# Kernel optimization log

Measured on AMD Instinct MI355X. Metric: run time of the kernel, lower is better.

The kernel has to match this reference:

```python
import jax, jax.numpy as jnp
import numpy as np

D_MODEL = 512; D_INNER = 1024; D_STATE = 16; DT_RANK = 32; D_CONV = 4
N_LAYERS = 2; LSPP = 7; N_ROI = 2048; HIDDEN = 4096


def layer_norm(x, g, b, eps=1e-5):
    mu = x.mean(-1, keepdims=True)
    v = ((x - mu) ** 2).mean(-1, keepdims=True)
    return (x - mu) * jax.lax.rsqrt(v + eps) * g + b


def causal_dwconv(u, w, b):
    # u: [N,L,Di], w: [Di,K] depthwise, causal left-pad K-1
    x = jnp.transpose(u, (0, 2, 1))
    out = jax.lax.conv_general_dilated(x, w[:, None, :], (1,), [(D_CONV - 1, 0)],
                                       dimension_numbers=('NCH', 'OIH', 'NCH'),
                                       feature_group_count=D_INNER)
    return jnp.transpose(out, (0, 2, 1)) + b


def selective_scan(u, dt, A, B, C):
    # u, dt: [N,L,Di]; B, C: [N,L,S]; A: [Di,S]
    def step(h, xs):
        dt_t, B_t, C_t, u_t = xs
        dA = jnp.exp(dt_t[..., None] * A)                      # [N,Di,S]
        h = dA * h + (dt_t * u_t)[..., None] * B_t[:, None, :]
        return h, jnp.einsum('nds,ns->nd', h, C_t)
    h0 = jnp.zeros((u.shape[0], D_INNER, D_STATE), u.dtype)
    xs = (jnp.moveaxis(dt, 1, 0), jnp.moveaxis(B, 1, 0),
          jnp.moveaxis(C, 1, 0), jnp.moveaxis(u, 1, 0))
    _, ys = jax.lax.scan(step, h0, xs)
    return jnp.moveaxis(ys, 0, 1)                              # [N,L,Di]


def mamba_block(h, inw, cw, cb, xpw, dtw, dtb, Alog, Dp, ow):
    # decomposed bidirectional mamba ('dbm'): shared in_proj/gate, fwd+bwd scans summed
    xz = h @ inw.T                                             # [N,L,2*Di]
    xi, z = jnp.split(xz, 2, axis=-1)
    ys = []
    for d in range(2):
        u = xi if d == 0 else jnp.flip(xi, axis=1)
        u = jax.nn.silu(causal_dwconv(u, cw[d], cb[d]))
        dbl = u @ xpw[d].T                                     # [N,L,DT_RANK+2S]
        dtr = dbl[..., :DT_RANK]
        B = dbl[..., DT_RANK:DT_RANK + D_STATE]
        C = dbl[..., DT_RANK + D_STATE:]
        dt = jax.nn.softplus(dtr @ dtw[d].T + dtb[d])
        A = -jnp.exp(Alog[d])
        yd = selective_scan(u, dt, A, B, C) + u * Dp[d]
        ys.append(yd if d == 0 else jnp.flip(yd, axis=1))
    return ((ys[0] + ys[1]) * jax.nn.silu(z)) @ ow.T


def setup_inputs() -> dict:
    key = jax.random.key(0)
    ks = iter(jax.random.split(key, 40))
    rn = lambda shape, scale: jax.random.normal(next(ks), shape, dtype=jnp.float32) * scale
    inp = {}
    inp['x_flat'] = rn((N_ROI, D_MODEL * LSPP), 1.0)
    inp['conv_a_w'] = rn((256, 512, 3), (512 * 3) ** -0.5)
    inp['conv_p_w'] = rn((256, 512, 1), 512 ** -0.5)
    inp['se_w1'] = rn((32, 512), 512 ** -0.5)
    inp['se_b1'] = jnp.zeros((32,), jnp.float32)
    inp['se_w2'] = rn((512, 32), 32 ** -0.5)
    inp['se_b2'] = jnp.zeros((512,), jnp.float32)
    inp['ln_g'] = jnp.ones((N_LAYERS, D_MODEL), jnp.float32)
    inp['ln_b'] = jnp.zeros((N_LAYERS, D_MODEL), jnp.float32)
    inp['in_proj_w'] = rn((N_LAYERS, 2 * D_INNER, D_MODEL), D_MODEL ** -0.5)
    inp['conv_w'] = rn((N_LAYERS, 2, D_INNER, D_CONV), D_CONV ** -0.5)
    inp['conv_b'] = jnp.zeros((N_LAYERS, 2, D_INNER), jnp.float32)
    inp['x_proj_w'] = rn((N_LAYERS, 2, DT_RANK + 2 * D_STATE, D_INNER), D_INNER ** -0.5)
    inp['dt_proj_w'] = rn((N_LAYERS, 2, D_INNER, DT_RANK), DT_RANK ** -0.5)
    inp['dt_proj_b'] = rn((N_LAYERS, 2, D_INNER), 0.1) - 4.0
    inp['A_log'] = jnp.log(jnp.arange(1., D_STATE + 1., dtype=jnp.float32)) * jnp.ones((N_LAYERS, 2, D_INNER, D_STATE), jnp.float32)
    inp['D_param'] = jnp.ones((N_LAYERS, 2, D_INNER), jnp.float32)
    inp['out_proj_w'] = rn((N_LAYERS, D_MODEL, D_INNER), D_INNER ** -0.5)
    inp['out_ln_g'] = jnp.ones((D_MODEL,), jnp.float32)
    inp['out_ln_b'] = jnp.zeros((D_MODEL,), jnp.float32)
    inp['mlp_w1'] = rn((HIDDEN, D_MODEL), D_MODEL ** -0.5)
    inp['mlp_b1'] = jnp.zeros((HIDDEN,), jnp.float32)
    inp['mlp_w2'] = rn((HIDDEN, HIDDEN), HIDDEN ** -0.5)
    inp['mlp_b2'] = jnp.zeros((HIDDEN,), jnp.float32)
    return inp


def reference(x_flat, conv_a_w, conv_p_w, se_w1, se_b1, se_w2, se_b2, ln_g, ln_b,
              in_proj_w, conv_w, conv_b, x_proj_w, dt_proj_w, dt_proj_b, A_log,
              D_param, out_proj_w, out_ln_g, out_ln_b, mlp_w1, mlp_b1, mlp_w2, mlp_b2):
    N = x_flat.shape[0]
    x = x_flat.reshape(N, D_MODEL, LSPP)                       # [N,512,7]
    dn = ('NCH', 'OIH', 'NCH')
    # TSSE: strided conv branch + maxpool branch, concat, SE gating; L: 7 -> 4
    a = jax.nn.relu(jax.lax.conv_general_dilated(x, conv_a_w, (2,), [(1, 1)], dimension_numbers=dn))
    p = jax.lax.reduce_window(x, -jnp.inf, jax.lax.max, (1, 1, 3), (1, 1, 2), ((0, 0), (0, 0), (1, 1)))
    p = jax.nn.relu(jax.lax.conv_general_dilated(p, conv_p_w, (1,), [(0, 0)], dimension_numbers=dn))
    y = jnp.concatenate([a, p], axis=1)                        # [N,512,4]
    s = jax.nn.sigmoid(jax.nn.relu(y.mean(-1) @ se_w1.T + se_b1) @ se_w2.T + se_b2)
    y = y * s[:, :, None]
    # Mamba backbone: 2 pre-norm residual DBM blocks (mask is all-ones -> no-op)
    h = jnp.transpose(y, (0, 2, 1))                            # [N,L,512]
    for l in range(N_LAYERS):
        h = h + mamba_block(layer_norm(h, ln_g[l], ln_b[l]), in_proj_w[l], conv_w[l],
                            conv_b[l], x_proj_w[l], dt_proj_w[l], dt_proj_b[l],
                            A_log[l], D_param[l], out_proj_w[l])
    h = layer_norm(h, out_ln_g, out_ln_b)
    feat = h.mean(1)                                           # mean pool over time
    z1 = jax.nn.relu(feat @ mlp_w1.T + mlp_b1)
    return jax.nn.relu(z1 @ mlp_w2.T + mlp_b2)                 # [N,4096]
```

## Files before the change

kernel.cpp:

```cpp
#include <hip/hip_runtime.h>
#include <hip/hip_bf16.h>

typedef __hip_bfloat16 bf16;
typedef __attribute__((ext_vector_type(8))) short s16x8;
typedef __attribute__((ext_vector_type(4))) float f32x4;

__device__ __forceinline__ float u2f(unsigned short u){
  union { unsigned int i; float f; } v; v.i = ((unsigned int)u) << 16; return v.f;
}
__device__ __forceinline__ float bfu(bf16 x){ return __bfloat162float(x); }
__device__ __forceinline__ bf16  f2b(float x){ return __float2bfloat16(x); }

__device__ __forceinline__ void gload16(const void* g, void* l){
  __builtin_amdgcn_global_load_lds(
      (const __attribute__((address_space(1))) void*)g,
      (__attribute__((address_space(3))) void*)l, 16, 0, 0);
}

__device__ __forceinline__ float block_sum256(float v, float* red){
  #pragma unroll
  for (int o = 32; o > 0; o >>= 1) v += __shfl_down(v, o, 64);
  int lane = threadIdx.x & 63, wid = threadIdx.x >> 6;
  if (lane == 0) red[wid] = v;
  __syncthreads();
  float r = red[0] + red[1] + red[2] + red[3];
  __syncthreads();
  return r;
}

__device__ __forceinline__ ushort4 cvt4(float4 v){
  ushort4 o;
  o.x = __bfloat16_as_ushort(f2b(v.x));
  o.y = __bfloat16_as_ushort(f2b(v.y));
  o.z = __bfloat16_as_ushort(f2b(v.z));
  o.w = __bfloat16_as_ushort(f2b(v.w));
  return o;
}

__global__ __launch_bounds__(256) void prep_kernel(
    const float* __restrict__ caw, const float* __restrict__ cpw,
    const float* __restrict__ ipw, const float* __restrict__ opw,
    const float* __restrict__ xpw, const float* __restrict__ dtw,
    const float* __restrict__ alog,
    bf16* __restrict__ wa, bf16* __restrict__ wp,
    bf16* __restrict__ wbi, bf16* __restrict__ wbo,
    bf16* __restrict__ wxp, bf16* __restrict__ wdtp,
    float* __restrict__ atab)
{
  for (int i = blockIdx.x*256 + threadIdx.x; i < 1769472; i += gridDim.x*256){
    if (i < 917504){
      int j = i;
      const float4* src; ushort4* dst;
      if (j < 98304)      { src = (const float4*)caw; dst = (ushort4*)wa; }
      else if (j < 131072){ j -= 98304;  src = (const float4*)cpw; dst = (ushort4*)wp; }
      else if (j < 655360){ j -= 131072; src = (const float4*)ipw; dst = (ushort4*)wbi; }
      else                { j -= 655360; src = (const float4*)opw; dst = (ushort4*)wbo; }
      dst[j] = cvt4(src[j]);
    } else if (i < 1441792){
      int idx = i - 917504;
      int l = idx >> 18, rem = idx & 262143, row = rem >> 10, c = rem & 1023;
      int d = row >> 7, r = row & 127;
      float v = (r < 64) ? xpw[(((size_t)l*2 + d)*64 + r)*1024 + c] : 0.f;
      wxp[idx] = f2b(v);
    } else if (i < 1703936){
      int idx = i - 1441792;
      int ld = idx >> 16, rem = idx & 65535, r = rem >> 6, cc = rem & 63;
      float v = (cc < 32) ? dtw[((size_t)ld*1024 + r)*32 + cc] : 0.f;
      wdtp[idx] = f2b(v);
    } else {
      int idx = i - 1703936;
      atab[idx] = -__expf(alog[idx]) * 1.44269504088896f;
    }
  }
}

__global__ __launch_bounds__(256) void mlpprep_kernel(
    const float4* __restrict__ w1, const float4* __restrict__ w2,
    ushort4* __restrict__ o1, ushort4* __restrict__ o2)
{
  for (int i = blockIdx.x*256 + threadIdx.x; i < 4718592; i += gridDim.x*256){
    if (i < 524288) o1[i] = cvt4(w1[i]);
    else            o2[i - 524288] = cvt4(w2[i - 524288]);
  }
}

template<int ACT, int OMODE, bool HASBIAS>
__global__ __launch_bounds__(256) void mgemm_kernel(
    const bf16* __restrict__ A, const bf16* __restrict__ W,
    const float* __restrict__ bias, void* __restrict__ outp,
    int K, int ldo)
{
  __shared__ char lsA[16384];
  __shared__ char lsB[16384];
  const int tid = threadIdx.x;
  const int w = tid >> 6, l = tid & 63;
  const int nwg = gridDim.x * gridDim.y;
  const int lin = blockIdx.y * gridDim.x + blockIdx.x;
  const int cpx = nwg >> 3;
  const int swz = (lin & 7) * cpx + (lin >> 3);
  const int m0 = (swz % gridDim.x) * 128, n0 = (swz / gridDim.x) * 128;
  const int wr = w >> 1, wc = w & 1;
  const size_t ldb = (size_t)K * 2;
  const char* Ab = (const char*)A + (size_t)m0 * ldb;
  const char* Wb = (const char*)W + (size_t)n0 * ldb;

  const int srow = l >> 3;
  const int scb  = ((l & 7) ^ srow) << 4;
  const int fr = l & 15;
  const int fg = l >> 4;
  const int fsw = (fr & 7) << 4;

  f32x4 acc[4][4];
  #pragma unroll
  for (int m = 0; m < 4; ++m)
    #pragma unroll
    for (int n = 0; n < 4; ++n) acc[m][n] = (f32x4){0.f,0.f,0.f,0.f};

  const int nk = K >> 6;
  for (int kt = 0; kt < nk; ++kt){
    const char* As = Ab + (size_t)kt * 128;
    const char* Ws = Wb + (size_t)kt * 128;
    #pragma unroll
    for (int i = 0; i < 4; ++i){
      int row = (i*4 + w)*8 + srow;
      gload16(As + (size_t)row*ldb + scb, &lsA[(i*4 + w)*1024]);
    }
    #pragma unroll
    for (int i = 0; i < 4; ++i){
      int row = (i*4 + w)*8 + srow;
      gload16(Ws + (size_t)row*ldb + scb, &lsB[(i*4 + w)*1024]);
    }
    __syncthreads();

    s16x8 af[4][2], bfr[4][2];
    #pragma unroll
    for (int m = 0; m < 4; ++m){
      int row = wr*64 + m*16 + fr;
      af[m][0] = *(const s16x8*)&lsA[row*128 + (( 0 + fg*16) ^ fsw)];
      af[m][1] = *(const s16x8*)&lsA[row*128 + ((64 + fg*16) ^ fsw)];
    }
    #pragma unroll
    for (int n = 0; n < 4; ++n){
      int row = wc*64 + n*16 + fr;
      bfr[n][0] = *(const s16x8*)&lsB[row*128 + (( 0 + fg*16) ^ fsw)];
      bfr[n][1] = *(const s16x8*)&lsB[row*128 + ((64 + fg*16) ^ fsw)];
    }
    #pragma unroll
    for (int m = 0; m < 4; ++m)
      #pragma unroll
      for (int n = 0; n < 4; ++n){
        acc[m][n] = __builtin_amdgcn_mfma_f32_16x16x32_bf16(af[m][0], bfr[n][0], acc[m][n], 0, 0, 0);
        acc[m][n] = __builtin_amdgcn_mfma_f32_16x16x32_bf16(af[m][1], bfr[n][1], acc[m][n], 0, 0, 0);
      }
    __syncthreads();
  }

  const int orow0 = m0 + wr*64, ocol0 = n0 + wc*64;
  #pragma unroll
  for (int n = 0; n < 4; ++n){
    int col = ocol0 + n*16 + fr;
    float bv = HASBIAS ? bias[col] : 0.f;
    #pragma unroll
    for (int m = 0; m < 4; ++m){
      int rbase = orow0 + m*16 + fg*4;
      #pragma unroll
      for (int r = 0; r < 4; ++r){
        float v = acc[m][n][r] + bv;
        if (ACT == 1) v = fmaxf(v, 0.f);
        if (ACT == 2) v = (v > 20.f) ? v : log1pf(__expf(v));
        size_t oi = (size_t)(rbase + r) * ldo + col;
        if (OMODE == 0)      ((bf16*)outp)[oi] = f2b(v);
        else if (OMODE == 1) ((float*)outp)[oi] = v;
        else                 ((float*)outp)[oi] += v;
      }
    }
  }
}

__global__ __launch_bounds__(256) void bgemm2_kernel(
    const bf16* __restrict__ xz, const bf16* __restrict__ W,
    const float* __restrict__ cw, const float* __restrict__ cb,
    bf16* __restrict__ dtr_buf, float* __restrict__ dbl)
{
  __shared__ char lsA[16384];
  __shared__ char lsB[16384];
  const int tid = threadIdx.x;
  const int w = tid >> 6, l = tid & 63;
  const int nwg = gridDim.x * 2;
  const int lin = blockIdx.y * gridDim.x + blockIdx.x;
  const int cpx = nwg >> 3;
  const int swz = (lin & 7) * cpx + (lin >> 3);
  const int m0 = (swz % gridDim.x) * 128;
  const int d  = swz / gridDim.x;
  const int K = 1024;
  const int wr = w >> 1, wc = w & 1;
  const size_t ldb = (size_t)K * 2;
  const char* Wb = (const char*)(W + (size_t)d*131072);
  const float* cwd = cw + d*4096;
  const float* cbd = cb + d*1024;
  const int n_base = m0 >> 2;

  const int srow = l >> 3;
  const int scb  = ((l & 7) ^ srow) << 4;
  const int fr = l & 15;
  const int fg = l >> 4;
  const int fsw = (fr & 7) << 4;

  const int a_n  = tid >> 3;
  const int a_j8 = tid & 7;

  f32x4 acc[4][4];
  #pragma unroll
  for (int m = 0; m < 4; ++m)
    #pragma unroll
    for (int n = 0; n < 4; ++n) acc[m][n] = (f32x4){0.f,0.f,0.f,0.f};

  for (int kt = 0; kt < 16; ++kt){
    const int ch = kt*64 + a_j8*8;
    s16x8 xr[4];
    #pragma unroll
    for (int tp = 0; tp < 4; ++tp)
      xr[tp] = *(const s16x8*)&xz[((size_t)(n_base + a_n)*4 + tp)*2048 + ch];
    s16x8 ot[4];
    #pragma unroll
    for (int jj = 0; jj < 8; ++jj){
      float xv[4];
      #pragma unroll
      for (int tp = 0; tp < 4; ++tp) xv[tp] = u2f((unsigned short)xr[tp][jj]);
      float xa[4];
      #pragma unroll
      for (int tp = 0; tp < 4; ++tp) xa[tp] = d ? xv[3-tp] : xv[tp];
      float4 w4 = *(const float4*)&cwd[(ch + jj)*4];
      float bb = cbd[ch + jj];
      float o[4];
      o[0] = xa[0]*w4.w + bb;
      o[1] = xa[0]*w4.z + xa[1]*w4.w + bb;
      o[2] = xa[0]*w4.y + xa[1]*w4.z + xa[2]*w4.w + bb;
      o[3] = xa[0]*w4.x + xa[1]*w4.y + xa[2]*w4.z + xa[3]*w4.w + bb;
      #pragma unroll
      for (int t = 0; t < 4; ++t){
        float v = o[t];
        float sv = v / (1.f + __expf(-v));
        ot[t][jj] = (short)__bfloat16_as_ushort(f2b(sv));
      }
    }
    #pragma unroll
    for (int t = 0; t < 4; ++t){
      int row = a_n*4 + t;
      *(s16x8*)&lsA[row*128 + ((a_j8 << 4) ^ ((row & 7) << 4))] = ot[t];
    }
    const char* Ws = Wb + (size_t)kt * 128;
    #pragma unroll
    for (int i = 0; i < 4; ++i){
      int row = (i*4 + w)*8 + srow;
      gload16(Ws + (size_t)row*ldb + scb, &lsB[(i*4 + w)*1024]);
    }
    __syncthreads();

    s16x8 af[4][2], bfr[4][2];
    #pragma unroll
    for (int m = 0; m < 4; ++m){
      int row = wr*64 + m*16 + fr;
      af[m][0] = *(const s16x8*)&lsA[row*128 + (( 0 + fg*16) ^ fsw)];
      af[m][1] = *(const s16x8*)&lsA[row*128 + ((64 + fg*16) ^ fsw)];
    }
    #pragma unroll
    for (int n = 0; n < 4; ++n){
      int row = wc*64 + n*16 + fr;
      bfr[n][0] = *(const s16x8*)&lsB[row*128 + (( 0 + fg*16) ^ fsw)];
      bfr[n][1] = *(const s16x8*)&lsB[row*128 + ((64 + fg*16) ^ fsw)];
    }
    #pragma unroll
    for (int m = 0; m < 4; ++m)
      #pragma unroll
      for (int n = 0; n < 4; ++n){
        acc[m][n] = __builtin_amdgcn_mfma_f32_16x16x32_bf16(af[m][0], bfr[n][0], acc[m][n], 0, 0, 0);
        acc[m][n] = __builtin_amdgcn_mfma_f32_16x16x32_bf16(af[m][1], bfr[n][1], acc[m][n], 0, 0, 0);
      }
    __syncthreads();
  }

  const int orow0 = m0 + wr*64, c0 = wc*64;
  #pragma unroll
  for (int n = 0; n < 4; ++n){
    int col = c0 + n*16 + fr;
    #pragma unroll
    for (int m = 0; m < 4; ++m){
      int rbase = orow0 + m*16 + fg*4;
      #pragma unroll
      for (int r = 0; r < 4; ++r){
        float v = acc[m][n][r];
        int row = rbase + r;
        if (col < 32)
          dtr_buf[((size_t)d*8192 + row)*64 + col] = f2b(v);
        else if (col < 64)
          dbl[(size_t)row*128 + d*64 + (col - 32)] = v;
        else if (col < 96)
          dtr_buf[((size_t)d*8192 + row)*64 + (col - 32)] = f2b(v);
      }
    }
  }
}

__global__ __launch_bounds__(256) void dtgemm_kernel(
    const bf16* __restrict__ A, const bf16* __restrict__ W2,
    const float* __restrict__ bias2, bf16* __restrict__ out2)
{
  __shared__ char lsA[16384];
  __shared__ char lsB[16384];
  const int tid = threadIdx.x;
  const int w = tid >> 6, l = tid & 63;
  const int nwg = gridDim.x * gridDim.y;
  const int lin = blockIdx.y * gridDim.x + blockIdx.x;
  const int cpx = nwg >> 3;
  const int swz = (lin & 7) * cpx + (lin >> 3);
  const int m0 = (swz % gridDim.x) * 128, n0 = (swz / gridDim.x) * 128;
  const int d  = (m0 >= 8192) ? 1 : 0;
  const int wr = w >> 1, wc = w & 1;
  const size_t ldb = 128;
  const char* Ab = (const char*)A + (size_t)m0 * ldb;
  const char* Wb = (const char*)(W2 + (size_t)d*65536) + (size_t)n0 * ldb;
  const float* bias = bias2 + d*1024;
  bf16* outp = out2 + (size_t)d*8388608;

  const int srow = l >> 3;
  const int scb  = ((l & 7) ^ srow) << 4;
  const int fr = l & 15, fg = l >> 4;
  const int fsw = (fr & 7) << 4;

  f32x4 acc[4][4];
  #pragma unroll
  for (int m = 0; m < 4; ++m)
    #pragma unroll
    for (int n = 0; n < 4; ++n) acc[m][n] = (f32x4){0.f,0.f,0.f,0.f};

  #pragma unroll
  for (int i = 0; i < 4; ++i){
    int row = (i*4 + w)*8 + srow;
    gload16(Ab + (size_t)row*ldb + scb, &lsA[(i*4 + w)*1024]);
  }
  #pragma unroll
  for (int i = 0; i < 4; ++i){
    int row = (i*4 + w)*8 + srow;
    gload16(Wb + (size_t)row*ldb + scb, &lsB[(i*4 + w)*1024]);
  }
  __syncthreads();

  s16x8 af[4][2], bfr[4][2];
  #pragma unroll
  for (int m = 0; m < 4; ++m){
    int row = wr*64 + m*16 + fr;
    af[m][0] = *(const s16x8*)&lsA[row*128 + (( 0 + fg*16) ^ fsw)];
    af[m][1] = *(const s16x8*)&lsA[row*128 + ((64 + fg*16) ^ fsw)];
  }
  #pragma unroll
  for (int n = 0; n < 4; ++n){
    int row = wc*64 + n*16 + fr;
    bfr[n][0] = *(const s16x8*)&lsB[row*128 + (( 0 + fg*16) ^ fsw)];
    bfr[n][1] = *(const s16x8*)&lsB[row*128 + ((64 + fg*16) ^ fsw)];
  }
  #pragma unroll
  for (int m = 0; m < 4; ++m)
    #pragma unroll
    for (int n = 0; n < 4; ++n){
      acc[m][n] = __builtin_amdgcn_mfma_f32_16x16x32_bf16(af[m][0], bfr[n][0], acc[m][n], 0, 0, 0);
      acc[m][n] = __builtin_amdgcn_mfma_f32_16x16x32_bf16(af[m][1], bfr[n][1], acc[m][n], 0, 0, 0);
    }

  const int orow0 = (m0 - d*8192) + wr*64, ocol0 = n0 + wc*64;
  #pragma unroll
  for (int n = 0; n < 4; ++n){
    int col = ocol0 + n*16 + fr;
    float bv = bias[col];
    #pragma unroll
    for (int m = 0; m < 4; ++m){
      int rbase = orow0 + m*16 + fg*4;
      #pragma unroll
      for (int r = 0; r < 4; ++r){
        float v = acc[m][n][r] + bv;
        v = (v > 20.f) ? v : log1pf(__expf(v));
        outp[(size_t)(rbase + r) * 1024 + col] = f2b(v);
      }
    }
  }
}

__global__ __launch_bounds__(256) void im2col_kernel(
    const float* __restrict__ x_flat, bf16* __restrict__ Aa, bf16* __restrict__ P)
{
  __shared__ float xs[512][8];
  const int n = blockIdx.x, tid = threadIdx.x;
  const float* xr = x_flat + (size_t)n * 3584;
  for (int i = tid; i < 3584; i += 256) xs[i / 7][i % 7] = xr[i];
  __syncthreads();
  bf16* Ar = Aa + (size_t)n * 4 * 1536;
  for (int i = tid; i < 6144; i += 256){
    int t = i / 1536, col = i - t*1536;
    int c = col / 3, kk = col - c*3;
    int p = 2*t - 1 + kk;
    float v = (p >= 0 && p < 7) ? xs[c][p] : 0.f;
    Ar[i] = f2b(v);
  }
  bf16* Pr = P + (size_t)n * 4 * 512;
  for (int i = tid; i < 2048; i += 256){
    int t = i >> 9, c = i & 511;
    int st = 2*t - 1;
    float m = -1e30f;
    #pragma unroll
    for (int k = 0; k < 3; ++k){ int p = st + k; if (p >= 0 && p < 7) m = fmaxf(m, xs[c][p]); }
    Pr[i] = f2b(m);
  }
}

__global__ __launch_bounds__(256) void se_kernel(
    const float* __restrict__ sw1, const float* __restrict__ sb1,
    const float* __restrict__ sw2, const float* __restrict__ sb2,
    float* __restrict__ h)
{
  __shared__ float yms[512];
  __shared__ float s1s[32];
  const int n = blockIdx.x, tid = threadIdx.x;
  float* hb = h + (size_t)n * 2048;
  for (int c = tid; c < 512; c += 256)
    yms[c] = 0.25f * (hb[c] + hb[512+c] + hb[1024+c] + hb[1536+c]);
  __syncthreads();
  {
    int o = tid >> 3, sl = tid & 7;
    const float* wr = sw1 + (size_t)o * 512 + sl*64;
    const float* ym = yms + sl*64;
    float a = 0.f;
    #pragma unroll 16
    for (int i = 0; i < 64; ++i) a += wr[i] * ym[i];
    a += __shfl_down(a, 4, 8);
    a += __shfl_down(a, 2, 8);
    a += __shfl_down(a, 1, 8);
    if (sl == 0) s1s[o] = fmaxf(a + sb1[o], 0.f);
  }
  __syncthreads();
  for (int c = tid; c < 512; c += 256){
    float a = sb2[c];
    const float* wr = sw2 + (size_t)c * 32;
    #pragma unroll
    for (int j = 0; j < 32; ++j) a += wr[j] * s1s[j];
    float s = 1.f / (1.f + __expf(-a));
    #pragma unroll
    for (int t = 0; t < 4; ++t) hb[t*512 + c] *= s;
  }
}

__global__ __launch_bounds__(256) void ln_kernel(
    const float* __restrict__ x, const float* __restrict__ g,
    const float* __restrict__ b, bf16* __restrict__ out)
{
  __shared__ float red[4];
  const int row = blockIdx.x, t = threadIdx.x;
  const float* xr = x + (size_t)row * 512;
  float v0 = xr[t], v1 = xr[t + 256];
  float s = block_sum256(v0 + v1, red);
  float mu = s * (1.f/512.f);
  float d0 = v0 - mu, d1 = v1 - mu;
  float sq = block_sum256(d0*d0 + d1*d1, red);
  float rstd = rsqrtf(sq * (1.f/512.f) + 1e-5f);
  out[(size_t)row*512 + t]       = f2b(d0*rstd*g[t]     + b[t]);
  out[(size_t)row*512 + t + 256] = f2b(d1*rstd*g[t+256] + b[t+256]);
}

__global__ __launch_bounds__(256) void finalln_kernel(
    const float* __restrict__ h, const float* __restrict__ g,
    const float* __restrict__ b, bf16* __restrict__ feat)
{
  __shared__ float red[4];
  const int n = blockIdx.x, t = threadIdx.x;
  float a0 = 0.f, a1 = 0.f;
  for (int tt = 0; tt < 4; ++tt){
    const float* xr = h + ((size_t)n*4 + tt)*512;
    float v0 = xr[t], v1 = xr[t+256];
    float s = block_sum256(v0 + v1, red);
    float mu = s * (1.f/512.f);
    float d0 = v0 - mu, d1 = v1 - mu;
    float sq = block_sum256(d0*d0 + d1*d1, red);
    float rstd = rsqrtf(sq * (1.f/512.f) + 1e-5f);
    a0 += d0*rstd*g[t]     + b[t];
    a1 += d1*rstd*g[t+256] + b[t+256];
  }
  feat[(size_t)n*512 + t]       = f2b(a0 * 0.25f);
  feat[(size_t)n*512 + t + 256] = f2b(a1 * 0.25f);
}

__global__ __launch_bounds__(256) void scan2_kernel(
    const float* __restrict__ dbl, const bf16* __restrict__ dt2,
    const bf16* __restrict__ xz, const float* __restrict__ cw,
    const float* __restrict__ cb, const float* __restrict__ Atab2,
    const float* __restrict__ Dp, bf16* __restrict__ gated)
{
  __shared__ float Bs[2][4][16], Cs[2][4][16];
  const int n = blockIdx.x, g = blockIdx.y, tid = threadIdx.x;
  {
    int t = tid >> 6, j = tid & 63;
    int d = j >> 5, jj = j & 31;
    float v = dbl[((size_t)n*4 + t)*128 + d*64 + jj];
    if (jj < 16) Bs[d][t][jj] = v; else Cs[d][t][jj-16] = v;
  }
  __syncthreads();
  const int c = g*256 + tid;
  const size_t base = (size_t)n*4*1024 + c;
  float xv[4];
  #pragma unroll
  for (int t = 0; t < 4; ++t) xv[t] = bfu(xz[((size_t)(n*4 + t))*2048 + c]);
  float4 w0 = *(const float4*)&cw[(size_t)c*4];
  float4 w1 = *(const float4*)&cw[4096 + (size_t)c*4];
  float b0v = cb[c], b1v = cb[1024 + c];
  float uu0[4], uu1[4];
  uu0[0] = xv[0]*w0.w + b0v;
  uu0[1] = xv[0]*w0.z + xv[1]*w0.w + b0v;
  uu0[2] = xv[0]*w0.y + xv[1]*w0.z + xv[2]*w0.w + b0v;
  uu0[3] = xv[0]*w0.x + xv[1]*w0.y + xv[2]*w0.z + xv[3]*w0.w + b0v;
  uu1[0] = xv[3]*w1.w + b1v;
  uu1[1] = xv[3]*w1.z + xv[2]*w1.w + b1v;
  uu1[2] = xv[3]*w1.y + xv[2]*w1.z + xv[1]*w1.w + b1v;
  uu1[3] = xv[3]*w1.x + xv[2]*w1.y + xv[1]*w1.z + xv[0]*w1.w + b1v;
  #pragma unroll
  for (int t = 0; t < 4; ++t){
    uu0[t] = uu0[t] / (1.f + __expf(-uu0[t]));
    uu1[t] = uu1[t] / (1.f + __expf(-uu1[t]));
  }
  float yo0[4], yo1[4];
  float hs[16];
  {
    float A[16];
    const float4* ap = reinterpret_cast<const float4*>(Atab2 + (size_t)c*16);
    #pragma unroll
    for (int q = 0; q < 4; ++q){
      float4 v = ap[q];
      A[q*4+0]=v.x; A[q*4+1]=v.y; A[q*4+2]=v.z; A[q*4+3]=v.w;
    }
    const float Dpc = Dp[c];
    #pragma unroll
    for (int s = 0; s < 16; ++s) hs[s] = 0.f;
    #pragma unroll
    for (int t = 0; t < 4; ++t){
      float dtv = bfu(dt2[base + (size_t)t*1024]);
      float du = dtv * uu0[t];
      float yv = 0.f;
      #pragma unroll
      for (int s = 0; s < 16; ++s){
        float dA = __builtin_amdgcn_exp2f(dtv * A[s]);
        hs[s] = dA * hs[s] + du * Bs[0][t][s];
        yv += hs[s] * Cs[0][t][s];
      }
      yo0[t] = yv + uu0[t] * Dpc;
    }
  }
  {
    float A[16];
    const float4* ap = reinterpret_cast<const float4*>(Atab2 + 16384 + (size_t)c*16);
    #pragma unroll
    for (int q = 0; q < 4; ++q){
      float4 v = ap[q];
      A[q*4+0]=v.x; A[q*4+1]=v.y; A[q*4+2]=v.z; A[q*4+3]=v.w;
    }
    const float Dpc = Dp[1024 + c];
    #pragma unroll
    for (int s = 0; s < 16; ++s) hs[s] = 0.f;
    #pragma unroll
    for (int t = 0; t < 4; ++t){
      float dtv = bfu(dt2[8388608 + base + (size_t)t*1024]);
      float du = dtv * uu1[t];
      float yv = 0.f;
      #pragma unroll
      for (int s = 0; s < 16; ++s){
        float dA = __builtin_amdgcn_exp2f(dtv * A[s]);
        hs[s] = dA * hs[s] + du * Bs[1][t][s];
        yv += hs[s] * Cs[1][t][s];
      }
      yo1[3 - t] = yv + uu1[t] * Dpc;
    }
  }
  #pragma unroll
  for (int t = 0; t < 4; ++t){
    float z = bfu(xz[(size_t)(n*4 + t)*2048 + 1024 + c]);
    float sv = z / (1.f + __expf(-z));
    gated[base + (size_t)t*1024] = f2b((yo0[t] + yo1[t]) * sv);
  }
}

extern "C" void kernel_launch(void* const* d_in, const int* in_sizes, int n_in,
                              void* d_out, int out_size, void* d_ws, size_t ws_size,
                              hipStream_t stream)
{
  const float* x_flat    = (const float*)d_in[0];
  const float* conv_a_w  = (const float*)d_in[1];
  const float* conv_p_w  = (const float*)d_in[2];
  const float* se_w1     = (const float*)d_in[3];
  const float* se_b1     = (const float*)d_in[4];
  const float* se_w2     = (const float*)d_in[5];
  const float* se_b2     = (const float*)d_in[6];
  const float* ln_g      = (const float*)d_in[7];
  const float* ln_b      = (const float*)d_in[8];
  const float* in_proj_w = (const float*)d_in[9];
  const float* conv_w    = (const float*)d_in[10];
  const float* conv_b    = (const float*)d_in[11];
  const float* x_proj_w  = (const float*)d_in[12];
  const float* dt_proj_w = (const float*)d_in[13];
  const float* dt_proj_b = (const float*)d_in[14];
  const float* A_log     = (const float*)d_in[15];
  const float* D_param   = (const float*)d_in[16];
  const float* out_proj_w= (const float*)d_in[17];
  const float* out_ln_g  = (const float*)d_in[18];
  const float* out_ln_b  = (const float*)d_in[19];
  const float* mlp_w1    = (const float*)d_in[20];
  const float* mlp_b1    = (const float*)d_in[21];
  const float* mlp_w2    = (const float*)d_in[22];
  const float* mlp_b2    = (const float*)d_in[23];

  char* ws = (char*)d_ws;
  const size_t OFF_H    = 0;
  const size_t OFF_HN   = OFF_H    + 16777216;
  const size_t OFF_XZ   = OFF_HN   + 8388608;
  const size_t OFF_U    = OFF_XZ   + 33554432;
  const size_t OFF_SCR  = OFF_U    + 33554432;
  const size_t OFF_YB   = OFF_SCR  + 25165824;
  const size_t OFF_WB   = OFF_YB   + 33554432;
  const size_t OFF_WXP  = OFF_WB   + 6291456;
  const size_t OFF_WDT  = OFF_WXP  + 1048576;
  const size_t OFF_ATAB = OFF_WDT  + 524288;

  float* h    = (float*)(ws + OFF_H);
  bf16*  hn   = (bf16*) (ws + OFF_HN);
  bf16*  xz   = (bf16*) (ws + OFF_XZ);
  bf16*  gated= (bf16*) (ws + OFF_U);
  float* dbl  = (float*)(ws + OFF_SCR);
  bf16*  dtrb = (bf16*) (ws + OFF_SCR + 4194304);
  bf16*  dt2  = (bf16*) (ws + OFF_YB);
  bf16*  feat = (bf16*) (ws + OFF_HN);
  bf16*  z1   = (bf16*) (ws + OFF_XZ);
  bf16*  wbi  = (bf16*) (ws + OFF_WB);
  bf16*  wbo  = (bf16*) (ws + OFF_WB + 4194304);
  bf16*  wxp  = (bf16*) (ws + OFF_WXP);
  bf16*  wdtp = (bf16*) (ws + OFF_WDT);
  float* Atab = (float*)(ws + OFF_ATAB);
  bf16*  wb1  = (bf16*) (ws + OFF_SCR);
  bf16*  wb2  = (bf16*) (ws + OFF_YB);
  bf16*  Aa   = (bf16*) (ws + OFF_SCR);
  bf16*  Pm   = (bf16*) (ws + OFF_YB);
  bf16*  wa   = (bf16*) (ws + OFF_YB + 8388608);
  bf16*  wp   = (bf16*) (ws + OFF_YB + 8388608 + 786432);
  float* outf = (float*)d_out;

  prep_kernel<<<2048, 256, 0, stream>>>(
      conv_a_w, conv_p_w, in_proj_w, out_proj_w, x_proj_w, dt_proj_w, A_log,
      wa, wp, wbi, wbo, wxp, wdtp, Atab);

  im2col_kernel<<<2048, 256, 0, stream>>>(x_flat, Aa, Pm);
  mgemm_kernel<1,1,false><<<dim3(64,2), 256, 0, stream>>>(
      Aa, wa, nullptr, h, 1536, 512);
  mgemm_kernel<1,1,false><<<dim3(64,2), 256, 0, stream>>>(
      Pm, wp, nullptr, (float*)h + 256, 512, 512);
  se_kernel<<<2048, 256, 0, stream>>>(se_w1, se_b1, se_w2, se_b2, h);

  for (int l = 0; l < 2; ++l){
    const float* cw_l = conv_w + (size_t)l*8192;
    const float* cb_l = conv_b + (size_t)l*2048;
    ln_kernel<<<8192, 256, 0, stream>>>(h, ln_g + l*512, ln_b + l*512, hn);
    mgemm_kernel<0,0,false><<<dim3(64,16), 256, 0, stream>>>(
        hn, wbi + (size_t)l*2048*512, nullptr, xz, 512, 2048);
    bgemm2_kernel<<<dim3(64,2), 256, 0, stream>>>(
        xz, wxp + (size_t)l*262144, cw_l, cb_l, dtrb, dbl);
    dtgemm_kernel<<<dim3(128,8), 256, 0, stream>>>(
        dtrb, wdtp + (size_t)l*131072, dt_proj_b + (size_t)l*2048, dt2);
    scan2_kernel<<<dim3(2048,4), 256, 0, stream>>>(
        dbl, dt2, xz, cw_l, cb_l, Atab + (size_t)l*32768,
        D_param + (size_t)l*2048, gated);
    mgemm_kernel<0,2,false><<<dim3(64,4), 256, 0, stream>>>(
        gated, wbo + (size_t)l*512*1024, nullptr, h, 1024, 512);
  }

  finalln_kernel<<<2048, 256, 0, stream>>>(h, out_ln_g, out_ln_b, feat);

  mlpprep_kernel<<<4096, 256, 0, stream>>>(
      (const float4*)mlp_w1, (const float4*)mlp_w2, (ushort4*)wb1, (ushort4*)wb2);

  mgemm_kernel<1,0,true><<<dim3(16,32), 256, 0, stream>>>(
      feat, wb1, mlp_b1, z1, 512, 4096);
  mgemm_kernel<1,1,true><<<dim3(16,32), 256, 0, stream>>>(
      z1, wb2, mlp_b2, outf, 4096, 4096);
}
```

Before: 715.3 us.

## Split depthwise conv into its own kernel and materialize u for GEMM and scan

Takes the causal depthwise conv plus SiLU out of the x_proj GEMM prologue and out of the scan. A new dwconv2 kernel computes both directions once and writes them to a bf16 buffer. The x_proj GEMM then streams that buffer straight into LDS with async global-to-LDS loads, and the scan reads u instead of recomputing it. This removes the redundant conv math and the per-k-tile ALU work from the low-occupancy GEMM, at the cost of an extra write and reads of a large intermediate buffer. The scan output also aliases the u buffer it reads.

```diff
diff --git a/kernel.cpp b/kernel.cpp
--- a/kernel.cpp
+++ b/kernel.cpp
@@ -177,9 +177,8 @@
   }
 }
 
-__global__ __launch_bounds__(256) void bgemm2_kernel(
-    const bf16* __restrict__ xz, const bf16* __restrict__ W,
-    const float* __restrict__ cw, const float* __restrict__ cb,
+__global__ __launch_bounds__(256) void bgemm_kernel(
+    const bf16* __restrict__ A, const bf16* __restrict__ W,
     bf16* __restrict__ dtr_buf, float* __restrict__ dbl)
 {
   __shared__ char lsA[16384];
@@ -195,10 +194,8 @@
   const int K = 1024;
   const int wr = w >> 1, wc = w & 1;
   const size_t ldb = (size_t)K * 2;
+  const char* Ab = (const char*)(A + (size_t)d*8388608) + (size_t)m0 * ldb;
   const char* Wb = (const char*)(W + (size_t)d*131072);
-  const float* cwd = cw + d*4096;
-  const float* cbd = cb + d*1024;
-  const int n_base = m0 >> 2;
 
   const int srow = l >> 3;
   const int scb  = ((l & 7) ^ srow) << 4;
@@ -206,50 +203,21 @@
   const int fg = l >> 4;
   const int fsw = (fr & 7) << 4;
 
-  const int a_n  = tid >> 3;
-  const int a_j8 = tid & 7;
-
   f32x4 acc[4][4];
   #pragma unroll
   for (int m = 0; m < 4; ++m)
     #pragma unroll
     for (int n = 0; n < 4; ++n) acc[m][n] = (f32x4){0.f,0.f,0.f,0.f};
 
-  for (int kt = 0; kt < 16; ++kt){
-    const int ch = kt*64 + a_j8*8;
-    s16x8 xr[4];
-    #pragma unroll
-    for (int tp = 0; tp < 4; ++tp)
-      xr[tp] = *(const s16x8*)&xz[((size_t)(n_base + a_n)*4 + tp)*2048 + ch];
-    s16x8 ot[4];
-    #pragma unroll
-    for (int jj = 0; jj < 8; ++jj){
-      float xv[4];
-      #pragma unroll
-      for (int tp = 0; tp < 4; ++tp) xv[tp] = u2f((unsigned short)xr[tp][jj]);
-      float xa[4];
-      #pragma unroll
-      for (int tp = 0; tp < 4; ++tp) xa[tp] = d ? xv[3-tp] : xv[tp];
-      float4 w4 = *(const float4*)&cwd[(ch + jj)*4];
-      float bb = cbd[ch + jj];
-      float o[4];
-      o[0] = xa[0]*w4.w + bb;
-      o[1] = xa[0]*w4.z + xa[1]*w4.w + bb;
-      o[2] = xa[0]*w4.y + xa[1]*w4.z + xa[2]*w4.w + bb;
-      o[3] = xa[0]*w4.x + xa[1]*w4.y + xa[2]*w4.z + xa[3]*w4.w + bb;
-      #pragma unroll
-      for (int t = 0; t < 4; ++t){
-        float v = o[t];
-        float sv = v / (1.f + __expf(-v));
-        ot[t][jj] = (short)__bfloat16_as_ushort(f2b(sv));
-      }
-    }
-    #pragma unroll
-    for (int t = 0; t < 4; ++t){
-      int row = a_n*4 + t;
-      *(s16x8*)&lsA[row*128 + ((a_j8 << 4) ^ ((row & 7) << 4))] = ot[t];
-    }
+  const int nk = K >> 6;
+  for (int kt = 0; kt < nk; ++kt){
+    const char* As = Ab + (size_t)kt * 128;
     const char* Ws = Wb + (size_t)kt * 128;
+    #pragma unroll
+    for (int i = 0; i < 4; ++i){
+      int row = (i*4 + w)*8 + srow;
+      gload16(As + (size_t)row*ldb + scb, &lsA[(i*4 + w)*1024]);
+    }
     #pragma unroll
     for (int i = 0; i < 4; ++i){
       int row = (i*4 + w)*8 + srow;
@@ -487,11 +455,57 @@
   feat[(size_t)n*512 + t + 256] = f2b(a1 * 0.25f);
 }
 
+__global__ __launch_bounds__(256) void dwconv2_kernel(
+    const bf16* __restrict__ xz, const float* __restrict__ cw,
+    const float* __restrict__ cb, bf16* __restrict__ u)
+{
+  const int n = blockIdx.x;
+  const int c4 = threadIdx.x * 4;
+  ushort4 in4[4];
+  #pragma unroll
+  for (int t = 0; t < 4; ++t)
+    in4[t] = *reinterpret_cast<const ushort4*>(&xz[((size_t)n*4 + t)*2048 + c4]);
+  #pragma unroll
+  for (int d = 0; d < 2; ++d){
+    const float* cwd = cw + d*4096;
+    const float* cbd = cb + d*1024;
+    ushort4 out[4];
+    #pragma unroll
+    for (int j = 0; j < 4; ++j){
+      float xa[4];
+      #pragma unroll
+      for (int t = 0; t < 4; ++t){
+        int ts = d ? 3 - t : t;
+        unsigned short us = j==0?in4[ts].x : j==1?in4[ts].y : j==2?in4[ts].z : in4[ts].w;
+        xa[t] = u2f(us);
+      }
+      float4 wv = *reinterpret_cast<const float4*>(&cwd[(c4 + j)*4]);
+      float bb = cbd[c4 + j];
+      float o[4];
+      o[0] = xa[0]*wv.w + bb;
+      o[1] = xa[0]*wv.z + xa[1]*wv.w + bb;
+      o[2] = xa[0]*wv.y + xa[1]*wv.z + xa[2]*wv.w + bb;
+      o[3] = xa[0]*wv.x + xa[1]*wv.y + xa[2]*wv.z + xa[3]*wv.w + bb;
+      #pragma unroll
+      for (int t = 0; t < 4; ++t){
+        float v = o[t];
+        float sv = v / (1.f + __expf(-v));
+        unsigned short us = __bfloat16_as_ushort(f2b(sv));
+        if (j==0) out[t].x = us; else if (j==1) out[t].y = us;
+        else if (j==2) out[t].z = us; else out[t].w = us;
+      }
+    }
+    #pragma unroll
+    for (int t = 0; t < 4; ++t)
+      *reinterpret_cast<ushort4*>(&u[(size_t)d*8388608 + ((size_t)n*4 + t)*1024 + c4]) = out[t];
+  }
+}
+
 __global__ __launch_bounds__(256) void scan2_kernel(
     const float* __restrict__ dbl, const bf16* __restrict__ dt2,
-    const bf16* __restrict__ xz, const float* __restrict__ cw,
-    const float* __restrict__ cb, const float* __restrict__ Atab2,
-    const float* __restrict__ Dp, bf16* __restrict__ gated)
+    const bf16* __restrict__ u, const bf16* __restrict__ xz,
+    const float* __restrict__ Atab2, const float* __restrict__ Dp,
+    bf16* __restrict__ gated)
 {
   __shared__ float Bs[2][4][16], Cs[2][4][16];
   const int n = blockIdx.x, g = blockIdx.y, tid = threadIdx.x;
@@ -504,26 +518,6 @@
   __syncthreads();
   const int c = g*256 + tid;
   const size_t base = (size_t)n*4*1024 + c;
-  float xv[4];
-  #pragma unroll
-  for (int t = 0; t < 4; ++t) xv[t] = bfu(xz[((size_t)(n*4 + t))*2048 + c]);
-  float4 w0 = *(const float4*)&cw[(size_t)c*4];
-  float4 w1 = *(const float4*)&cw[4096 + (size_t)c*4];
-  float b0v = cb[c], b1v = cb[1024 + c];
-  float uu0[4], uu1[4];
-  uu0[0] = xv[0]*w0.w + b0v;
-  uu0[1] = xv[0]*w0.z + xv[1]*w0.w + b0v;
-  uu0[2] = xv[0]*w0.y + xv[1]*w0.z + xv[2]*w0.w + b0v;
-  uu0[3] = xv[0]*w0.x + xv[1]*w0.y + xv[2]*w0.z + xv[3]*w0.w + b0v;
-  uu1[0] = xv[3]*w1.w + b1v;
-  uu1[1] = xv[3]*w1.z + xv[2]*w1.w + b1v;
-  uu1[2] = xv[3]*w1.y + xv[2]*w1.z + xv[1]*w1.w + b1v;
-  uu1[3] = xv[3]*w1.x + xv[2]*w1.y + xv[1]*w1.z + xv[0]*w1.w + b1v;
-  #pragma unroll
-  for (int t = 0; t < 4; ++t){
-    uu0[t] = uu0[t] / (1.f + __expf(-uu0[t]));
-    uu1[t] = uu1[t] / (1.f + __expf(-uu1[t]));
-  }
   float yo0[4], yo1[4];
   float hs[16];
   {
@@ -540,7 +534,8 @@
     #pragma unroll
     for (int t = 0; t < 4; ++t){
       float dtv = bfu(dt2[base + (size_t)t*1024]);
-      float du = dtv * uu0[t];
+      float uv  = bfu(u  [base + (size_t)t*1024]);
+      float du = dtv * uv;
       float yv = 0.f;
       #pragma unroll
       for (int s = 0; s < 16; ++s){
@@ -548,7 +543,7 @@
         hs[s] = dA * hs[s] + du * Bs[0][t][s];
         yv += hs[s] * Cs[0][t][s];
       }
-      yo0[t] = yv + uu0[t] * Dpc;
+      yo0[t] = yv + uv * Dpc;
     }
   }
   {
@@ -565,7 +560,8 @@
     #pragma unroll
     for (int t = 0; t < 4; ++t){
       float dtv = bfu(dt2[8388608 + base + (size_t)t*1024]);
-      float du = dtv * uu1[t];
+      float uv  = bfu(u  [8388608 + base + (size_t)t*1024]);
+      float du = dtv * uv;
       float yv = 0.f;
       #pragma unroll
       for (int s = 0; s < 16; ++s){
@@ -573,7 +569,7 @@
         hs[s] = dA * hs[s] + du * Bs[1][t][s];
         yv += hs[s] * Cs[1][t][s];
       }
-      yo1[3 - t] = yv + uu1[t] * Dpc;
+      yo1[3 - t] = yv + uv * Dpc;
     }
   }
   #pragma unroll
@@ -628,7 +624,7 @@
   float* h    = (float*)(ws + OFF_H);
   bf16*  hn   = (bf16*) (ws + OFF_HN);
   bf16*  xz   = (bf16*) (ws + OFF_XZ);
-  bf16*  gated= (bf16*) (ws + OFF_U);
+  bf16*  u    = (bf16*) (ws + OFF_U);
   float* dbl  = (float*)(ws + OFF_SCR);
   bf16*  dtrb = (bf16*) (ws + OFF_SCR + 4194304);
   bf16*  dt2  = (bf16*) (ws + OFF_YB);
@@ -659,20 +655,20 @@
   se_kernel<<<2048, 256, 0, stream>>>(se_w1, se_b1, se_w2, se_b2, h);
 
   for (int l = 0; l < 2; ++l){
-    const float* cw_l = conv_w + (size_t)l*8192;
-    const float* cb_l = conv_b + (size_t)l*2048;
     ln_kernel<<<8192, 256, 0, stream>>>(h, ln_g + l*512, ln_b + l*512, hn);
     mgemm_kernel<0,0,false><<<dim3(64,16), 256, 0, stream>>>(
         hn, wbi + (size_t)l*2048*512, nullptr, xz, 512, 2048);
-    bgemm2_kernel<<<dim3(64,2), 256, 0, stream>>>(
-        xz, wxp + (size_t)l*262144, cw_l, cb_l, dtrb, dbl);
+    dwconv2_kernel<<<2048, 256, 0, stream>>>(
+        xz, conv_w + (size_t)l*8192, conv_b + (size_t)l*2048, u);
+    bgemm_kernel<<<dim3(64,2), 256, 0, stream>>>(
+        u, wxp + (size_t)l*262144, dtrb, dbl);
     dtgemm_kernel<<<dim3(128,8), 256, 0, stream>>>(
         dtrb, wdtp + (size_t)l*131072, dt_proj_b + (size_t)l*2048, dt2);
     scan2_kernel<<<dim3(2048,4), 256, 0, stream>>>(
-        dbl, dt2, xz, cw_l, cb_l, Atab + (size_t)l*32768,
-        D_param + (size_t)l*2048, gated);
+        dbl, dt2, u, xz, Atab + (size_t)l*32768, D_param + (size_t)l*2048,
+        u );
     mgemm_kernel<0,2,false><<<dim3(64,4), 256, 0, stream>>>(
-        gated, wbo + (size_t)l*512*1024, nullptr, h, 1024, 512);
+        u, wbo + (size_t)l*512*1024, nullptr, h, 1024, 512);
   }
 
   finalln_kernel<<<2048, 256, 0, stream>>>(h, out_ln_g, out_ln_b, feat);
```

New measurement: 679.5 us. -5.0%, faster.
